# Optimization experiments

Hardware: AMD Instinct MI355X
Metric: run time of the kernel (lower is better)

The kernel has to match this reference:

```python
import jax, jax.numpy as jnp
import numpy as np

N, E, F_IN, C, H, G = 50000, 800000, 128, 64, 4, 512

def _gat_layer(x, src, dst, W, a_src, a_dst, b):
    # x: [N, Fin]; W: [Fin, H*C]; a_src/a_dst: [H, C]; b: [C]
    n = x.shape[0]
    h = (x @ W).reshape(n, H, C)                      # [N,H,C]
    al_s = jnp.einsum('nhc,hc->nh', h, a_src)         # [N,H]
    al_d = jnp.einsum('nhc,hc->nh', h, a_dst)
    alpha = jax.nn.leaky_relu(al_s[src] + al_d[dst], 0.2)   # [Et,H]
    m = jax.ops.segment_max(alpha, dst, num_segments=n)      # segment softmax over dst
    e = jnp.exp(alpha - m[dst])
    s = jax.ops.segment_sum(e, dst, num_segments=n)
    coef = e / (s[dst] + 1e-16)                        # [Et,H]
    msg = h[src] * coef[:, :, None]                    # [Et,H,C]
    out = jax.ops.segment_sum(msg, dst, num_segments=n)
    return out.mean(axis=1) + b                        # concat=False: average heads

def setup_inputs():
    key = jax.random.key(0)
    ks = jax.random.split(key, 24)
    x = jax.random.normal(ks[0], (N, F_IN), jnp.float32)
    edge_index = jax.random.randint(ks[1], (2, E), 0, N, jnp.int64)
    edge_attr = jax.random.normal(ks[2], (E, 4), jnp.float32)
    batch_index = jnp.sort(jax.random.randint(ks[3], (N,), 0, G, jnp.int64))
    p = lambda k, shp: jax.random.normal(k, shp, jnp.float32) * 0.05
    inp = {
        'x': x, 'edge_index': edge_index, 'edge_attr': edge_attr, 'batch_index': batch_index,
        'W0': p(ks[4], (F_IN, H * C)), 'as0': p(ks[5], (H, C)), 'ad0': p(ks[6], (H, C)), 'b0': jnp.zeros((C,), jnp.float32),
        'W1': p(ks[7], (C, H * C)), 'as1': p(ks[8], (H, C)), 'ad1': p(ks[9], (H, C)), 'b1': jnp.zeros((C,), jnp.float32),
        'W2': p(ks[10], (C, H * C)), 'as2': p(ks[11], (H, C)), 'ad2': p(ks[12], (H, C)), 'b2': jnp.zeros((C,), jnp.float32),
        'Wr1': p(ks[13], (2 * C, C)), 'br1': jnp.zeros((C,), jnp.float32),
        'Wr2': p(ks[14], (C, 1)), 'br2': jnp.zeros((1,), jnp.float32),
    }
    return inp

def reference(x, edge_index, edge_attr, batch_index,
              W0, as0, ad0, b0, W1, as1, ad1, b1, W2, as2, ad2, b2,
              Wr1, br1, Wr2, br2):
    # add self-loops (PyG GATConv default add_self_loops=True); edge_attr unused (edge_dim=None)
    loop = jnp.arange(N, dtype=edge_index.dtype)
    src = jnp.concatenate([edge_index[0], loop])
    dst = jnp.concatenate([edge_index[1], loop])
    h = jax.nn.leaky_relu(_gat_layer(x, src, dst, W0, as0, ad0, b0))
    h = jax.nn.leaky_relu(_gat_layer(h, src, dst, W1, as1, ad1, b1))
    h = jax.nn.leaky_relu(_gat_layer(h, src, dst, W2, as2, ad2, b2))
    gmp = jax.ops.segment_max(h, batch_index, num_segments=G)           # [G,C]
    cnt = jax.ops.segment_sum(jnp.ones((N,), h.dtype), batch_index, num_segments=G)
    gap = jax.ops.segment_sum(h, batch_index, num_segments=G) / jnp.maximum(cnt, 1.0)[:, None]
    hid = jnp.concatenate([gmp, gap], axis=1)                            # [G,2C]
    hid = jax.nn.leaky_relu(hid @ Wr1 + br1)
    return hid @ Wr2 + br2                                               # [G,1]
```

## Files before the change

kernel.cpp:

```cpp
#include <hip/hip_runtime.h>
#include <hip/hip_bf16.h>
#include <hip/hip_fp16.h>

#define NN   50000
#define EE   800000
#define FIN  128
#define CC   64
#define HH   4
#define GG   512
#define CAP  64

typedef _Float16 f16x8 __attribute__((ext_vector_type(8)));
typedef float    f32x4 __attribute__((ext_vector_type(4)));

__device__ __forceinline__ float leaky02(float x) { return x >= 0.f ? x : 0.2f * x; }
__device__ __forceinline__ float leaky01(float x) { return x >= 0.f ? x : 0.01f * x; }

__global__ __launch_bounds__(256) void build_csr(const int* __restrict__ ei,
                                                 int* __restrict__ deg,
                                                 int* __restrict__ csr) {
    int e = blockIdx.x * 256 + threadIdx.x;
    if (e >= EE) return;
    int s = ei[e];
    int d = ei[EE + e];
    if ((unsigned)d >= NN || (unsigned)s >= NN) return;
    int pos = atomicAdd(&deg[d], 1);
    if (pos < CAP) csr[d * CAP + pos] = s;
}

__global__ __launch_bounds__(256) void convert_x(const float* __restrict__ x,
                                                 __half* __restrict__ xh,
                                                 __half* __restrict__ xl,
                                                 int n) {
    int i = (blockIdx.x * 256 + threadIdx.x) * 8;
    if (i >= n) return;
    float v[8];
    *(float4*)&v[0] = *(const float4*)(x + i);
    *(float4*)&v[4] = *(const float4*)(x + i + 4);
    __half hi[8], lo[8];
#pragma unroll
    for (int j = 0; j < 8; ++j) {
        hi[j] = __float2half_rn(v[j]);
        lo[j] = __float2half_rn(v[j] - __half2float(hi[j]));
    }
    *(uint4*)(xh + i) = *(uint4*)hi;
    *(uint4*)(xl + i) = *(uint4*)lo;
}

__global__ __launch_bounds__(256) void convert_w(const float* __restrict__ W,
                                                 __half* __restrict__ wph,
                                                 __half* __restrict__ wpl,
                                                 int K) {
    int id = blockIdx.x * 256 + threadIdx.x;
    int total = (K / 32) * 16 * 64;
    if (id >= total) return;
    int lane = id & 63;
    int c    = (id >> 6) & 15;
    int kc   = id >> 10;
    int kbase = kc * 32 + (lane >> 4) * 8;
    int col   = c * 16 + (lane & 15);
    __half hi[8], lo[8];
#pragma unroll
    for (int j = 0; j < 8; ++j) {
        float v = W[(size_t)(kbase + j) * 256 + col];
        hi[j] = __float2half_rn(v);
        lo[j] = __float2half_rn(v - __half2float(hi[j]));
    }
    *(uint4*)(wph + (size_t)id * 8) = *(uint4*)hi;
    *(uint4*)(wpl + (size_t)id * 8) = *(uint4*)lo;
}

template <int K>
__global__ __launch_bounds__(256) void gemm_mfma(const __half* __restrict__ xh,
                                                 const __half* __restrict__ xl,
                                                 const __half* __restrict__ wph,
                                                 const __half* __restrict__ wpl,
                                                 const float* __restrict__ a_src,
                                                 const float* __restrict__ a_dst,
                                                 __half* __restrict__ h_out,
                                                 float* __restrict__ al_s,
                                                 float* __restrict__ al_d) {
    const int t    = threadIdx.x;
    const int w    = t >> 6;
    const int lane = t & 63;
    const int r0   = blockIdx.x * 64 + w * 16;
    const int colL = lane & 15;
    const int rowg = lane >> 4;
    int arow = r0 + colL;
    arow = arow < NN ? arow : NN - 1;
    const int koff = rowg * 8;

    f32x4 acc[16];
#pragma unroll
    for (int c = 0; c < 16; ++c) acc[c] = (f32x4){0.f, 0.f, 0.f, 0.f};

    for (int kc = 0; kc < K / 32; ++kc) {
        f16x8 ah = *(const f16x8*)(xh + (size_t)arow * K + kc * 32 + koff);
        f16x8 al = *(const f16x8*)(xl + (size_t)arow * K + kc * 32 + koff);
        const __half* bbase_h = wph + ((size_t)(kc * 16) * 64 + lane) * 8;
        const __half* bbase_l = wpl + ((size_t)(kc * 16) * 64 + lane) * 8;
#pragma unroll
        for (int c = 0; c < 16; ++c) {
            f16x8 bh = *(const f16x8*)(bbase_h + c * 512);
            f16x8 bl = *(const f16x8*)(bbase_l + c * 512);
            acc[c] = __builtin_amdgcn_mfma_f32_16x16x32_f16(ah, bh, acc[c], 0, 0, 0);
            acc[c] = __builtin_amdgcn_mfma_f32_16x16x32_f16(al, bh, acc[c], 0, 0, 0);
            acc[c] = __builtin_amdgcn_mfma_f32_16x16x32_f16(ah, bl, acc[c], 0, 0, 0);
        }
    }

    float aps[4][4], apd[4][4];
#pragma unroll
    for (int r = 0; r < 4; ++r)
#pragma unroll
        for (int h = 0; h < 4; ++h) { aps[r][h] = 0.f; apd[r][h] = 0.f; }

#pragma unroll
    for (int c = 0; c < 16; ++c) {
        const int col = c * 16 + colL;
        const float as = a_src[col];
        const float ad = a_dst[col];
        const int hh = c >> 2;
#pragma unroll
        for (int r = 0; r < 4; ++r) {
            const int row = r0 + rowg * 4 + r;
            const float v = acc[c][r];
            if (row < NN) h_out[(size_t)row * 256 + col] = __float2half_rn(v);
            aps[r][hh] = fmaf(v, as, aps[r][hh]);
            apd[r][hh] = fmaf(v, ad, apd[r][hh]);
        }
    }
#pragma unroll
    for (int r = 0; r < 4; ++r)
#pragma unroll
        for (int h = 0; h < 4; ++h) {
            float s = aps[r][h], d = apd[r][h];
#pragma unroll
            for (int off = 1; off <= 8; off <<= 1) {
                s += __shfl_xor(s, off, 64);
                d += __shfl_xor(d, off, 64);
            }
            aps[r][h] = s; apd[r][h] = d;
        }
    if (colL == 0) {
#pragma unroll
        for (int r = 0; r < 4; ++r) {
            const int row = r0 + rowg * 4 + r;
            if (row < NN) {
#pragma unroll
                for (int h = 0; h < 4; ++h) {
                    al_s[(size_t)row * 4 + h] = aps[r][h];
                    al_d[(size_t)row * 4 + h] = apd[r][h];
                }
            }
        }
    }
}

struct Half8 { __half2 h[4]; };

__global__ __launch_bounds__(256) void gat_aggregate(const __half* __restrict__ h_buf,
                                                     const float* __restrict__ al_s,
                                                     const float* __restrict__ al_d,
                                                     const int* __restrict__ deg,
                                                     const int* __restrict__ csr,
                                                     const float* __restrict__ bias,
                                                     __half* __restrict__ xb_hi,
                                                     __half* __restrict__ xb_lo) {
    __shared__ __align__(16) __half2 els[4][66][4];
    const int w    = threadIdx.x >> 6;
    const int lane = threadIdx.x & 63;
    const int n    = blockIdx.x * 4 + w;
    const int d = min(deg[n], CAP);

    float4 ad4 = *(const float4*)(al_d + (size_t)n * 4);
    float4 as4 = *(const float4*)(al_s + (size_t)n * 4);
    const float* adp = (const float*)&ad4;
    const float* asp = (const float*)&as4;

    float aself[4];
#pragma unroll
    for (int h = 0; h < 4; ++h) aself[h] = leaky02(asp[h] + adp[h]);

    int s_lane = 0;
    float a_lane[4];
    if (lane < d) {
        s_lane = csr[(size_t)n * CAP + lane];
        float4 s4 = *(const float4*)(al_s + (size_t)s_lane * 4);
        const float* sp = (const float*)&s4;
#pragma unroll
        for (int h = 0; h < 4; ++h) a_lane[h] = leaky02(sp[h] + adp[h]);
    } else {
#pragma unroll
        for (int h = 0; h < 4; ++h) a_lane[h] = -INFINITY;
    }

    float mx[4];
#pragma unroll
    for (int h = 0; h < 4; ++h) {
        mx[h] = fmaxf(aself[h], a_lane[h]);
#pragma unroll
        for (int off = 32; off; off >>= 1) mx[h] = fmaxf(mx[h], __shfl_xor(mx[h], off, 64));
    }

    float e[4], sm[4];
#pragma unroll
    for (int h = 0; h < 4; ++h) {
        e[h] = (lane < d) ? expf(a_lane[h] - mx[h]) : 0.f;
        sm[h] = e[h];
#pragma unroll
        for (int off = 32; off; off >>= 1) sm[h] += __shfl_xor(sm[h], off, 64);
    }
    float eself[4], inv[4];
#pragma unroll
    for (int h = 0; h < 4; ++h) {
        eself[h] = expf(aself[h] - mx[h]);
        inv[h] = 1.f / (sm[h] + eself[h] + 1e-16f);
    }
    if (lane < d) {
#pragma unroll
        for (int h = 0; h < 4; ++h) {
            float c = e[h] * inv[h];
            els[w][lane + 1][h] = __floats2half2_rn(c, c);
        }
    }
    if (lane == 0) {
#pragma unroll
        for (int h = 0; h < 4; ++h) {
            float c = eself[h] * inv[h];
            els[w][0][h] = __floats2half2_rn(c, c);
        }
    }

    const int q    = lane >> 5;
    const int m    = lane & 31;
    const int head = m >> 3;
    const __half* __restrict__ hb = h_buf + m * 8;

    __half2 z = __floats2half2_rn(0.f, 0.f);
    __half2 acc0 = z, acc1 = z, acc2 = z, acc3 = z;
    const int count = d + 1;
    for (int t2 = 0; 2 * t2 < count; ++t2) {
        int v = 2 * t2 + q;
        int vi = v > 0 ? v - 1 : 0;
        int s = __shfl(s_lane, vi, 64);
        s = v == 0 ? n : s;
        if (v < count) {
            __half2 c2 = els[w][v][head];
            Half8 r = *(const Half8*)(hb + (size_t)s * 256);
            acc0 = __hfma2(r.h[0], c2, acc0);
            acc1 = __hfma2(r.h[1], c2, acc1);
            acc2 = __hfma2(r.h[2], c2, acc2);
            acc3 = __hfma2(r.h[3], c2, acc3);
        }
    }

    int i0 = __shfl_xor(*(int*)&acc0, 32, 64);
    int i1 = __shfl_xor(*(int*)&acc1, 32, 64);
    int i2 = __shfl_xor(*(int*)&acc2, 32, 64);
    int i3 = __shfl_xor(*(int*)&acc3, 32, 64);
    acc0 = __hadd2(acc0, *(__half2*)&i0);
    acc1 = __hadd2(acc1, *(__half2*)&i1);
    acc2 = __hadd2(acc2, *(__half2*)&i2);
    acc3 = __hadd2(acc3, *(__half2*)&i3);

    float ch[8];
    float2 f;
    f = __half22float2(acc0); ch[0] = f.x; ch[1] = f.y;
    f = __half22float2(acc1); ch[2] = f.x; ch[3] = f.y;
    f = __half22float2(acc2); ch[4] = f.x; ch[5] = f.y;
    f = __half22float2(acc3); ch[6] = f.x; ch[7] = f.y;
#pragma unroll
    for (int k = 0; k < 8; ++k) {
        ch[k] += __shfl_xor(ch[k], 8, 64);
        ch[k] += __shfl_xor(ch[k], 16, 64);
    }
    if (lane < 8) {
        __align__(16) __half hi8[8], lo8[8];
#pragma unroll
        for (int k = 0; k < 8; ++k) {
            float o = leaky01(ch[k] * 0.25f + bias[lane * 8 + k]);
            __half hv = __float2half_rn(o);
            hi8[k] = hv;
            lo8[k] = __float2half_rn(o - __half2float(hv));
        }
        *(uint4*)(xb_hi + (size_t)n * 64 + lane * 8) = *(uint4*)hi8;
        *(uint4*)(xb_lo + (size_t)n * 64 + lane * 8) = *(uint4*)lo8;
    }
}

__global__ __launch_bounds__(256) void readout(const __half* __restrict__ x,
                                               const int* __restrict__ batch,
                                               float* __restrict__ gmp,
                                               float* __restrict__ gap) {
    int g = blockIdx.x;
    int a = 0, b = NN;
    while (a < b) { int m = (a + b) >> 1; if (batch[m] < g) a = m + 1; else b = m; }
    int lo = a;
    a = lo; b = NN;
    while (a < b) { int m = (a + b) >> 1; if (batch[m] < g + 1) a = m + 1; else b = m; }
    int hi = a;

    int t = threadIdx.x, c = t & 63, s = t >> 6;
    float mx = -INFINITY, sm = 0.f;
    for (int n = lo + s; n < hi; n += 4) {
        float v = __half2float(x[(size_t)n * 64 + c]);
        mx = fmaxf(mx, v);
        sm += v;
    }
    __shared__ float smx[256], ssm[256];
    smx[t] = mx; ssm[t] = sm;
    __syncthreads();
    if (t < 64) {
        mx = fmaxf(fmaxf(smx[t], smx[t + 64]), fmaxf(smx[t + 128], smx[t + 192]));
        sm = ssm[t] + ssm[t + 64] + ssm[t + 128] + ssm[t + 192];
        int cnt = hi - lo;
        gmp[g * 64 + t] = mx;
        gap[g * 64 + t] = sm / fmaxf((float)cnt, 1.0f);
    }
}

__global__ __launch_bounds__(64) void mlp_readout(const float* __restrict__ gmp,
                                                  const float* __restrict__ gap,
                                                  const float* __restrict__ Wr1,
                                                  const float* __restrict__ br1,
                                                  const float* __restrict__ Wr2,
                                                  const float* __restrict__ br2,
                                                  float* __restrict__ out) {
    int g = blockIdx.x;
    int j = threadIdx.x;
    double acc = (double)br1[j];
    for (int i = 0; i < 64; ++i) acc += (double)gmp[g * 64 + i] * (double)Wr1[i * 64 + j];
    for (int i = 0; i < 64; ++i) acc += (double)gap[g * 64 + i] * (double)Wr1[(64 + i) * 64 + j];
    float v = (float)acc;
    v = v >= 0.f ? v : 0.01f * v;
    double tv = (double)v * (double)Wr2[j];
#pragma unroll
    for (int off = 32; off; off >>= 1) tv += __shfl_xor(tv, off, 64);
    if (j == 0) out[g] = (float)(tv + (double)br2[0]);
}

extern "C" void kernel_launch(void* const* d_in, const int* in_sizes, int n_in,
                              void* d_out, int out_size, void* d_ws, size_t ws_size,
                              hipStream_t stream) {
    const float* x   = (const float*)d_in[0];
    const int* ei    = (const int*)d_in[1];
    const int* batch = (const int*)d_in[3];
    const float* W0  = (const float*)d_in[4];
    const float* as0 = (const float*)d_in[5];
    const float* ad0 = (const float*)d_in[6];
    const float* b0  = (const float*)d_in[7];
    const float* W1  = (const float*)d_in[8];
    const float* as1 = (const float*)d_in[9];
    const float* ad1 = (const float*)d_in[10];
    const float* b1  = (const float*)d_in[11];
    const float* W2  = (const float*)d_in[12];
    const float* as2 = (const float*)d_in[13];
    const float* ad2 = (const float*)d_in[14];
    const float* b2  = (const float*)d_in[15];
    const float* Wr1 = (const float*)d_in[16];
    const float* br1 = (const float*)d_in[17];
    const float* Wr2 = (const float*)d_in[18];
    const float* br2 = (const float*)d_in[19];
    float* out = (float*)d_out;

    __half* h_buf = (__half*)d_ws;
    __half* x_hi  = h_buf + (size_t)NN * 256;
    __half* x_lo  = x_hi + (size_t)NN * 128;
    __half* xb_hi = x_hi;
    __half* xb_lo = x_lo;
    __half* w0ph  = x_lo + (size_t)NN * 128;
    __half* w0pl  = w0ph + 32768;
    __half* w1ph  = w0pl + 32768;
    __half* w1pl  = w1ph + 16384;
    __half* w2ph  = w1pl + 16384;
    __half* w2pl  = w2ph + 16384;
    float*  al_s  = (float*)(w2pl + 16384);
    float*  al_d  = al_s + (size_t)NN * 4;
    float*  gmp   = al_d + (size_t)NN * 4;
    float*  gap   = gmp + (size_t)GG * 64;
    int*    deg   = (int*)(gap + (size_t)GG * 64);
    int*    csr   = deg + NN;

    hipMemsetAsync(deg, 0, NN * sizeof(int), stream);
    build_csr<<<(EE + 255) / 256, 256, 0, stream>>>(ei, deg, csr);

    convert_x<<<(NN * FIN / 8 + 255) / 256, 256, 0, stream>>>(x, x_hi, x_lo, NN * FIN);
    convert_w<<<16, 256, 0, stream>>>(W0, w0ph, w0pl, 128);
    convert_w<<<8, 256, 0, stream>>>(W1, w1ph, w1pl, 64);
    convert_w<<<8, 256, 0, stream>>>(W2, w2ph, w2pl, 64);

    const int gemm_grid = (NN + 63) / 64;
    const int agg_grid  = (NN + 3) / 4;

    gemm_mfma<FIN><<<gemm_grid, 256, 0, stream>>>(x_hi, x_lo, w0ph, w0pl, as0, ad0, h_buf, al_s, al_d);
    gat_aggregate<<<agg_grid, 256, 0, stream>>>(h_buf, al_s, al_d, deg, csr, b0, xb_hi, xb_lo);
    gemm_mfma<CC><<<gemm_grid, 256, 0, stream>>>(xb_hi, xb_lo, w1ph, w1pl, as1, ad1, h_buf, al_s, al_d);
    gat_aggregate<<<agg_grid, 256, 0, stream>>>(h_buf, al_s, al_d, deg, csr, b1, xb_hi, xb_lo);
    gemm_mfma<CC><<<gemm_grid, 256, 0, stream>>>(xb_hi, xb_lo, w2ph, w2pl, as2, ad2, h_buf, al_s, al_d);
    gat_aggregate<<<agg_grid, 256, 0, stream>>>(h_buf, al_s, al_d, deg, csr, b2, xb_hi, xb_lo);

    readout<<<GG, 256, 0, stream>>>(xb_hi, batch, gmp, gap);
    mlp_readout<<<GG, 64, 0, stream>>>(gmp, gap, Wr1, br1, Wr2, br2, out);
}
```

Before: 498.3 us.

## Fuse x conversion into GEMM, drop low-half activations, stage output via LDS

The separate fp32-to-fp16 split of x is removed and folded into the first GEMM, which now reads fp32 directly. Layers 1 and 2 keep only a single fp16 copy of the activations, so the aggregate kernel writes one buffer and the GEMM issues two MFMAs per tile instead of three. The three weight-conversion launches become one kernel, and the GEMM output goes through a swizzled shared-memory tile so global stores are 16-byte coalesced. Dropping the low-half activation term lowers precision in the later layers, and the new 32 KB shared buffer may reduce occupancy.

```diff
diff --git a/kernel.cpp b/kernel.cpp
--- a/kernel.cpp
+++ b/kernel.cpp
@@ -28,32 +28,18 @@
     if (pos < CAP) csr[d * CAP + pos] = s;
 }
 
-__global__ __launch_bounds__(256) void convert_x(const float* __restrict__ x,
-                                                 __half* __restrict__ xh,
-                                                 __half* __restrict__ xl,
-                                                 int n) {
-    int i = (blockIdx.x * 256 + threadIdx.x) * 8;
-    if (i >= n) return;
-    float v[8];
-    *(float4*)&v[0] = *(const float4*)(x + i);
-    *(float4*)&v[4] = *(const float4*)(x + i + 4);
-    __half hi[8], lo[8];
-#pragma unroll
-    for (int j = 0; j < 8; ++j) {
-        hi[j] = __float2half_rn(v[j]);
-        lo[j] = __float2half_rn(v[j] - __half2float(hi[j]));
-    }
-    *(uint4*)(xh + i) = *(uint4*)hi;
-    *(uint4*)(xl + i) = *(uint4*)lo;
-}
-
-__global__ __launch_bounds__(256) void convert_w(const float* __restrict__ W,
-                                                 __half* __restrict__ wph,
-                                                 __half* __restrict__ wpl,
-                                                 int K) {
-    int id = blockIdx.x * 256 + threadIdx.x;
-    int total = (K / 32) * 16 * 64;
-    if (id >= total) return;
+__global__ __launch_bounds__(256) void convert_w3(const float* __restrict__ W0,
+                                                  const float* __restrict__ W1,
+                                                  const float* __restrict__ W2,
+                                                  __half* __restrict__ w0ph, __half* __restrict__ w0pl,
+                                                  __half* __restrict__ w1ph, __half* __restrict__ w1pl,
+                                                  __half* __restrict__ w2ph, __half* __restrict__ w2pl) {
+    const float* W;
+    __half *wph, *wpl;
+    int id;
+    if (blockIdx.x < 16)      { W = W0; wph = w0ph; wpl = w0pl; id = blockIdx.x * 256 + threadIdx.x; }
+    else if (blockIdx.x < 24) { W = W1; wph = w1ph; wpl = w1pl; id = (blockIdx.x - 16) * 256 + threadIdx.x; }
+    else                      { W = W2; wph = w2ph; wpl = w2pl; id = (blockIdx.x - 24) * 256 + threadIdx.x; }
     int lane = id & 63;
     int c    = (id >> 6) & 15;
     int kc   = id >> 10;
@@ -70,9 +56,8 @@
     *(uint4*)(wpl + (size_t)id * 8) = *(uint4*)lo;
 }
 
-template <int K>
-__global__ __launch_bounds__(256) void gemm_mfma(const __half* __restrict__ xh,
-                                                 const __half* __restrict__ xl,
+template <int K, bool XF32>
+__global__ __launch_bounds__(256) void gemm_mfma(const void* __restrict__ xin,
                                                  const __half* __restrict__ wph,
                                                  const __half* __restrict__ wpl,
                                                  const float* __restrict__ a_src,
@@ -80,6 +65,7 @@
                                                  __half* __restrict__ h_out,
                                                  float* __restrict__ al_s,
                                                  float* __restrict__ al_d) {
+    __shared__ __half hst[4][16 * 256];
     const int t    = threadIdx.x;
     const int w    = t >> 6;
     const int lane = t & 63;
@@ -95,8 +81,22 @@
     for (int c = 0; c < 16; ++c) acc[c] = (f32x4){0.f, 0.f, 0.f, 0.f};
 
     for (int kc = 0; kc < K / 32; ++kc) {
-        f16x8 ah = *(const f16x8*)(xh + (size_t)arow * K + kc * 32 + koff);
-        f16x8 al = *(const f16x8*)(xl + (size_t)arow * K + kc * 32 + koff);
+        f16x8 ah, al;
+        if (XF32) {
+            const float* xf = (const float*)xin;
+            float v[8];
+            *(float4*)&v[0] = *(const float4*)(xf + (size_t)arow * K + kc * 32 + koff);
+            *(float4*)&v[4] = *(const float4*)(xf + (size_t)arow * K + kc * 32 + koff + 4);
+#pragma unroll
+            for (int j = 0; j < 8; ++j) {
+                float hi = (float)(_Float16)v[j];
+                ah[j] = (_Float16)v[j];
+                al[j] = (_Float16)(v[j] - hi);
+            }
+        } else {
+            const __half* xh = (const __half*)xin;
+            ah = *(const f16x8*)(xh + (size_t)arow * K + kc * 32 + koff);
+        }
         const __half* bbase_h = wph + ((size_t)(kc * 16) * 64 + lane) * 8;
         const __half* bbase_l = wpl + ((size_t)(kc * 16) * 64 + lane) * 8;
 #pragma unroll
@@ -104,8 +104,9 @@
             f16x8 bh = *(const f16x8*)(bbase_h + c * 512);
             f16x8 bl = *(const f16x8*)(bbase_l + c * 512);
             acc[c] = __builtin_amdgcn_mfma_f32_16x16x32_f16(ah, bh, acc[c], 0, 0, 0);
-            acc[c] = __builtin_amdgcn_mfma_f32_16x16x32_f16(al, bh, acc[c], 0, 0, 0);
             acc[c] = __builtin_amdgcn_mfma_f32_16x16x32_f16(ah, bl, acc[c], 0, 0, 0);
+            if (XF32)
+                acc[c] = __builtin_amdgcn_mfma_f32_16x16x32_f16(al, bh, acc[c], 0, 0, 0);
         }
     }
 
@@ -114,7 +115,6 @@
     for (int r = 0; r < 4; ++r)
 #pragma unroll
         for (int h = 0; h < 4; ++h) { aps[r][h] = 0.f; apd[r][h] = 0.f; }
-
 #pragma unroll
     for (int c = 0; c < 16; ++c) {
         const int col = c * 16 + colL;
@@ -123,11 +123,8 @@
         const int hh = c >> 2;
 #pragma unroll
         for (int r = 0; r < 4; ++r) {
-            const int row = r0 + rowg * 4 + r;
-            const float v = acc[c][r];
-            if (row < NN) h_out[(size_t)row * 256 + col] = __float2half_rn(v);
-            aps[r][hh] = fmaf(v, as, aps[r][hh]);
-            apd[r][hh] = fmaf(v, ad, apd[r][hh]);
+            aps[r][hh] = fmaf(acc[c][r], as, aps[r][hh]);
+            apd[r][hh] = fmaf(acc[c][r], ad, apd[r][hh]);
         }
     }
 #pragma unroll
@@ -152,6 +149,29 @@
                     al_s[(size_t)row * 4 + h] = aps[r][h];
                     al_d[(size_t)row * 4 + h] = apd[r][h];
                 }
+            }
+        }
+    }
+
+    __half* my = hst[w];
+#pragma unroll
+    for (int c = 0; c < 16; ++c) {
+        const int c16 = c * 2 + (colL >> 3);
+#pragma unroll
+        for (int r = 0; r < 4; ++r) {
+            const int rl = rowg * 4 + r;
+            my[rl * 256 + ((c16 ^ rl) * 8) + (colL & 7)] = __float2half_rn(acc[c][r]);
+        }
+    }
+    {
+        const int rl = lane >> 2;
+        const int row = r0 + rl;
+        if (row < NN) {
+#pragma unroll
+            for (int j = 0; j < 8; ++j) {
+                const int chunk = (lane & 3) * 8 + j;
+                uint4 v = *(const uint4*)&my[rl * 256 + ((chunk ^ rl) * 8)];
+                *(uint4*)(h_out + (size_t)row * 256 + chunk * 8) = v;
             }
         }
     }
@@ -165,8 +185,7 @@
                                                      const int* __restrict__ deg,
                                                      const int* __restrict__ csr,
                                                      const float* __restrict__ bias,
-                                                     __half* __restrict__ xb_hi,
-                                                     __half* __restrict__ xb_lo) {
+                                                     __half* __restrict__ xb) {
     __shared__ __align__(16) __half2 els[4][66][4];
     const int w    = threadIdx.x >> 6;
     const int lane = threadIdx.x & 63;
@@ -235,7 +254,7 @@
     const int q    = lane >> 5;
     const int m    = lane & 31;
     const int head = m >> 3;
-    const __half* __restrict__ hb = h_buf + m * 8;
+    const char* __restrict__ hb = (const char*)h_buf + m * 16;
 
     __half2 z = __floats2half2_rn(0.f, 0.f);
     __half2 acc0 = z, acc1 = z, acc2 = z, acc3 = z;
@@ -247,7 +266,7 @@
         s = v == 0 ? n : s;
         if (v < count) {
             __half2 c2 = els[w][v][head];
-            Half8 r = *(const Half8*)(hb + (size_t)s * 256);
+            Half8 r = *(const Half8*)(hb + (size_t)((unsigned)s << 9));
             acc0 = __hfma2(r.h[0], c2, acc0);
             acc1 = __hfma2(r.h[1], c2, acc1);
             acc2 = __hfma2(r.h[2], c2, acc2);
@@ -276,16 +295,11 @@
         ch[k] += __shfl_xor(ch[k], 16, 64);
     }
     if (lane < 8) {
-        __align__(16) __half hi8[8], lo8[8];
-#pragma unroll
-        for (int k = 0; k < 8; ++k) {
-            float o = leaky01(ch[k] * 0.25f + bias[lane * 8 + k]);
-            __half hv = __float2half_rn(o);
-            hi8[k] = hv;
-            lo8[k] = __float2half_rn(o - __half2float(hv));
-        }
-        *(uint4*)(xb_hi + (size_t)n * 64 + lane * 8) = *(uint4*)hi8;
-        *(uint4*)(xb_lo + (size_t)n * 64 + lane * 8) = *(uint4*)lo8;
+        __align__(16) __half h8[8];
+#pragma unroll
+        for (int k = 0; k < 8; ++k)
+            h8[k] = __float2half_rn(leaky01(ch[k] * 0.25f + bias[lane * 8 + k]));
+        *(uint4*)(xb + (size_t)n * 64 + lane * 8) = *(uint4*)h8;
     }
 }
 
@@ -365,11 +379,8 @@
     float* out = (float*)d_out;
 
     __half* h_buf = (__half*)d_ws;
-    __half* x_hi  = h_buf + (size_t)NN * 256;
-    __half* x_lo  = x_hi + (size_t)NN * 128;
-    __half* xb_hi = x_hi;
-    __half* xb_lo = x_lo;
-    __half* w0ph  = x_lo + (size_t)NN * 128;
+    __half* xb    = h_buf + (size_t)NN * 256;
+    __half* w0ph  = xb + (size_t)NN * 64;
     __half* w0pl  = w0ph + 32768;
     __half* w1ph  = w0pl + 32768;
     __half* w1pl  = w1ph + 16384;
@@ -384,22 +395,18 @@
 
     hipMemsetAsync(deg, 0, NN * sizeof(int), stream);
     build_csr<<<(EE + 255) / 256, 256, 0, stream>>>(ei, deg, csr);
-
-    convert_x<<<(NN * FIN / 8 + 255) / 256, 256, 0, stream>>>(x, x_hi, x_lo, NN * FIN);
-    convert_w<<<16, 256, 0, stream>>>(W0, w0ph, w0pl, 128);
-    convert_w<<<8, 256, 0, stream>>>(W1, w1ph, w1pl, 64);
-    convert_w<<<8, 256, 0, stream>>>(W2, w2ph, w2pl, 64);
+    convert_w3<<<32, 256, 0, stream>>>(W0, W1, W2, w0ph, w0pl, w1ph, w1pl, w2ph, w2pl);
 
     const int gemm_grid = (NN + 63) / 64;
     const int agg_grid  = (NN + 3) / 4;
 
-    gemm_mfma<FIN><<<gemm_grid, 256, 0, stream>>>(x_hi, x_lo, w0ph, w0pl, as0, ad0, h_buf, al_s, al_d);
-    gat_aggregate<<<agg_grid, 256, 0, stream>>>(h_buf, al_s, al_d, deg, csr, b0, xb_hi, xb_lo);
-    gemm_mfma<CC><<<gemm_grid, 256, 0, stream>>>(xb_hi, xb_lo, w1ph, w1pl, as1, ad1, h_buf, al_s, al_d);
-    gat_aggregate<<<agg_grid, 256, 0, stream>>>(h_buf, al_s, al_d, deg, csr, b1, xb_hi, xb_lo);
-    gemm_mfma<CC><<<gemm_grid, 256, 0, stream>>>(xb_hi, xb_lo, w2ph, w2pl, as2, ad2, h_buf, al_s, al_d);
-    gat_aggregate<<<agg_grid, 256, 0, stream>>>(h_buf, al_s, al_d, deg, csr, b2, xb_hi, xb_lo);
-
-    readout<<<GG, 256, 0, stream>>>(xb_hi, batch, gmp, gap);
+    gemm_mfma<FIN, true><<<gemm_grid, 256, 0, stream>>>(x, w0ph, w0pl, as0, ad0, h_buf, al_s, al_d);
+    gat_aggregate<<<agg_grid, 256, 0, stream>>>(h_buf, al_s, al_d, deg, csr, b0, xb);
+    gemm_mfma<CC, false><<<gemm_grid, 256, 0, stream>>>(xb, w1ph, w1pl, as1, ad1, h_buf, al_s, al_d);
+    gat_aggregate<<<agg_grid, 256, 0, stream>>>(h_buf, al_s, al_d, deg, csr, b1, xb);
+    gemm_mfma<CC, false><<<gemm_grid, 256, 0, stream>>>(xb, w2ph, w2pl, as2, ad2, h_buf, al_s, al_d);
+    gat_aggregate<<<agg_grid, 256, 0, stream>>>(h_buf, al_s, al_d, deg, csr, b2, xb);
+
+    readout<<<GG, 256, 0, stream>>>(xb, batch, gmp, gap);
     mlp_readout<<<GG, 64, 0, stream>>>(gmp, gap, Wr1, br1, Wr2, br2, out);
 }
```

Measured after the change: 478.3 us. 4.0% less time.
